# Kernel tuning notes

Measured on AMD Instinct MI355X. Metric: run time of the kernel, lower is better.

Reference implementation:

```python
import jax, jax.numpy as jnp
import numpy as np

M, N, T = 32, 32, 512
H1 = (M + N) * 10 * 8      # 5120
H2 = M * N * 4             # 4096
HID = 1000                 # GRU hidden (hardcoded in module)
EPS = 1e-12


def _l2norm(x):
    # torch.nn.functional.normalize: x / max(||x||_2, eps)
    return x / jnp.maximum(jnp.linalg.norm(x), EPS)


def setup_inputs() -> dict:
    key = jax.random.key(0)
    ks = jax.random.split(key, 16)
    rn = lambda k, shp, s: (jax.random.normal(k, shp, dtype=jnp.float32) * s)
    inp = {
        "y": rn(ks[0], (T, N), 1.0),
        "F": rn(ks[1], (M, M), 0.5 / np.sqrt(M)),   # stable dynamics
        "H": rn(ks[2], (N, M), 1.0 / np.sqrt(M)),
        "m1x0": rn(ks[3], (M,), 1.0),
        "h0": rn(ks[4], (HID,), 1.0),
        "W1": rn(ks[5], (H1, M + N), 1.0 / np.sqrt(M + N)),
        "b1": rn(ks[6], (H1,), 0.01),
        "Wih": rn(ks[7], (3 * HID, H1), 1.0 / np.sqrt(H1)),
        "bih": rn(ks[8], (3 * HID,), 0.01),
        "Whh": rn(ks[9], (3 * HID, HID), 1.0 / np.sqrt(HID)),
        "bhh": rn(ks[10], (3 * HID,), 0.01),
        "W2": rn(ks[11], (H2, HID), 1.0 / np.sqrt(HID)),
        "b2": rn(ks[12], (H2,), 0.01),
        "W3": rn(ks[13], (M * N, H2), 1.0 / np.sqrt(H2)),
        "b3": rn(ks[14], (M * N,), 0.01),
    }
    return inp


def reference(y, F, H, m1x0, h0, W1, b1, Wih, bih, Whh, bhh, W2, b2, W3, b3):
    m, n = F.shape[0], H.shape[0]

    def step(carry, yt):
        m1x_prior, m1x_post, h = carry
        # step_prior
        m1x_prev_prior = m1x_prior
        m1x_prior = F @ m1x_post              # [m]
        m1y = H @ m1x_prior                   # [n]
        # step_KGain_est: features
        dm1x_n = _l2norm(m1x_post - m1x_prev_prior)
        dm1y_n = _l2norm(yt - m1y)
        kin = jnp.concatenate([dm1y_n, dm1x_n])  # [n+m]
        # KGain_step: Linear+ReLU -> single-step GRU -> Linear+ReLU -> Linear
        x = jax.nn.relu(W1 @ kin + b1)        # [H1]
        gi = Wih @ x + bih                    # [3*HID]
        gh = Whh @ h + bhh
        ir, iz, ic = jnp.split(gi, 3)
        hr, hz, hc = jnp.split(gh, 3)
        r = jax.nn.sigmoid(ir + hr)
        z = jax.nn.sigmoid(iz + hz)
        c = jnp.tanh(ic + r * hc)
        h_new = (1.0 - z) * c + z * h         # GRU hidden [HID]
        l2 = jax.nn.relu(W2 @ h_new + b2)     # [H2]
        KG = (W3 @ l2 + b3).reshape(m, n)     # Kalman gain
        # KNet_step: innovation update
        m1x_post_new = m1x_prior + KG @ (yt - m1y)
        return (m1x_prior, m1x_post_new, h_new), m1x_post_new

    init = (m1x0, m1x0, h0)
    _, posts = jax.lax.scan(step, init, y)
    return posts  # [T, m]
```

## Files before the change

### kernel.cpp

```cpp
#include <hip/hip_runtime.h>
#include <cmath>

#define Mdim 32
#define Ndim 32
#define Tsteps 512
#define H1dim 5120
#define H2dim 4096
#define HIDdim 1000
#define NWG 256
#define NTHR 1024
#define POLLER 320

typedef unsigned int u32;
typedef unsigned short u16;
typedef unsigned int u32x4 __attribute__((ext_vector_type(4)));

__device__ u16 g_w2b[H2dim * HIDdim];
__device__ u16 g_w3t[H2dim * Mdim * Ndim];

#define OFF_WIH 0
#define OFF_WHH 122880
#define OFF_UNION 146880
#define OFF_H9 157120
#define OFF_MISC 161640
#define SMEM_BYTES 162560

#define MI_POST 0
#define MI_PRIOR 32
#define MI_INNOV 96
#define MI_KIN 128
#define MI_GI 192
#define MI_GH 204

__device__ __forceinline__ u16 f2bf(float f) {
  u32 u = __float_as_uint(f);
  return (u16)((u + 0x7fffu + ((u >> 16) & 1u)) >> 16);
}
__device__ __forceinline__ float bflo(u32 u) { return __uint_as_float(u << 16); }
__device__ __forceinline__ float bfhi(u32 u) { return __uint_as_float(u & 0xffff0000u); }

__device__ __forceinline__ float dot4(float4 a, float4 b) {
  return a.x * b.x + a.y * b.y + a.z * b.z + a.w * b.w;
}
__device__ __forceinline__ float dot8_bb(uint4 a, uint4 b) {
  float s = 0.f;
  s = fmaf(bflo(a.x), bflo(b.x), s); s = fmaf(bfhi(a.x), bfhi(b.x), s);
  s = fmaf(bflo(a.y), bflo(b.y), s); s = fmaf(bfhi(a.y), bfhi(b.y), s);
  s = fmaf(bflo(a.z), bflo(b.z), s); s = fmaf(bfhi(a.z), bfhi(b.z), s);
  s = fmaf(bflo(a.w), bflo(b.w), s); s = fmaf(bfhi(a.w), bfhi(b.w), s);
  return s;
}
__device__ __forceinline__ float dot8_bf(uint4 a, const float* x8) {
  float s = 0.f;
  s = fmaf(bflo(a.x), x8[0], s); s = fmaf(bfhi(a.x), x8[1], s);
  s = fmaf(bflo(a.y), x8[2], s); s = fmaf(bfhi(a.y), x8[3], s);
  s = fmaf(bflo(a.z), x8[4], s); s = fmaf(bfhi(a.z), x8[5], s);
  s = fmaf(bflo(a.w), x8[6], s); s = fmaf(bfhi(a.w), x8[7], s);
  return s;
}

__device__ __forceinline__ float wave_reduce64(float v) {
#pragma unroll
  for (int off = 32; off >= 1; off >>= 1) v += __shfl_xor(v, off, 64);
  return v;
}

__device__ __forceinline__ uint4 ldg_cg4u(const void* p) {
  uint4 r;
  asm volatile("global_load_dwordx4 %0, %1, off sc0 sc1\n\ts_waitcnt vmcnt(0)"
               : "=v"(r) : "v"(p) : "memory");
  return r;
}
__device__ __forceinline__ void ldg2_cg4(const float* p0, const float* p1,
                                         float4& r0, float4& r1) {
  asm volatile("global_load_dwordx4 %0, %2, off sc0 sc1\n\t"
               "global_load_dwordx4 %1, %3, off sc0 sc1\n\t"
               "s_waitcnt vmcnt(0)"
               : "=&v"(r0), "=&v"(r1) : "v"(p0), "v"(p1) : "memory");
}
__device__ __forceinline__ void stg_cg1(float* p, float v) {
  asm volatile("global_store_dword %0, %1, off sc0 sc1" :: "v"(p), "v"(v) : "memory");
}
__device__ __forceinline__ void stg_cg4u(void* p, u32 a, u32 b, u32 c, u32 d) {
  u32x4 v; v.x = a; v.y = b; v.z = c; v.w = d;
  asm volatile("global_store_dwordx4 %0, %1, off sc0 sc1" :: "v"(p), "v"(v) : "memory");
}

__device__ __forceinline__ void gb_arrive(u32* bar) {
  asm volatile("s_waitcnt vmcnt(0)" ::: "memory");
  __syncthreads();
  if (threadIdx.x == POLLER) {
    u32 g = (u32)blockIdx.x & 15u;
    u32 a = __hip_atomic_fetch_add(bar + g * 16, 1u, __ATOMIC_RELAXED,
                                   __HIP_MEMORY_SCOPE_AGENT);
    if ((a & 15u) == 15u) {
      u32 b = __hip_atomic_fetch_add(bar + 256, 1u, __ATOMIC_RELAXED,
                                     __HIP_MEMORY_SCOPE_AGENT);
      if ((b & 15u) == 15u)
        __hip_atomic_fetch_add(bar + 320, 1u, __ATOMIC_RELAXED,
                               __HIP_MEMORY_SCOPE_AGENT);
    }
  }
}
__device__ __forceinline__ void gb_wait(u32* bar, u32 nb) {
  if (threadIdx.x == POLLER) {
    while (__hip_atomic_load(bar + 320, __ATOMIC_RELAXED,
                             __HIP_MEMORY_SCOPE_AGENT) < nb)
      __builtin_amdgcn_s_sleep(2);
  }
  __syncthreads();
}

__global__ void convert_w2(const float* __restrict__ W2) {
  int i = blockIdx.x * 1024 + threadIdx.x;
  if (i < H2dim * HIDdim) g_w2b[i] = f2bf(W2[i]);
}

__global__ void convert_w3t(const float* __restrict__ W3) {
  __shared__ float tile[32][33];
  int tr = blockIdx.x >> 7;
  int tc = blockIdx.x & 127;
  int r0 = tr * 32, c0 = tc * 32;
  int j = threadIdx.x & 31, i0 = threadIdx.x >> 5;
#pragma unroll
  for (int p = 0; p < 4; ++p) {
    int i = i0 + p * 8;
    tile[i][j] = W3[(size_t)(r0 + i) * H2dim + c0 + j];
  }
  __syncthreads();
#pragma unroll
  for (int p = 0; p < 4; ++p) {
    int i = i0 + p * 8;
    g_w3t[(size_t)(c0 + i) * 1024 + r0 + j] = f2bf(tile[j][i]);
  }
}

__global__ void __launch_bounds__(NTHR)
knet_kernel(const float* __restrict__ y, const float* __restrict__ F,
            const float* __restrict__ Hm, const float* __restrict__ m1x0,
            const float* __restrict__ h0, const float* __restrict__ W1,
            const float* __restrict__ b1, const float* __restrict__ Wih,
            const float* __restrict__ bih, const float* __restrict__ Whh,
            const float* __restrict__ bhh, const float* __restrict__ b2,
            const float* __restrict__ b3, float* __restrict__ out,
            u32* bar, u32* xbt, u32* hbt, float* dpart) {
  extern __shared__ char smem[];
  u16* s_wih = (u16*)(smem + OFF_WIH);
  u16* s_whh = (u16*)(smem + OFF_WHH);
  u16* s_x = (u16*)(smem + OFF_UNION);
  float4* s_red4 = (float4*)(smem + OFF_UNION);
  float* s_redf = (float*)(smem + OFF_UNION);
  float* s_pd = (float*)(smem + OFF_UNION);
  float* s_h9 = (float*)(smem + OFF_H9);
  float* s_m = (float*)(smem + OFF_MISC);
  float* s_post = s_m + MI_POST;
  float* s_prior = s_m + MI_PRIOR;
  float* s_innov = s_m + MI_INNOV;
  float* s_kin = s_m + MI_KIN;
  float* s_gi = s_m + MI_GI;
  float* s_gh = s_m + MI_GH;

  const int tid = threadIdx.x;
  const int w = tid >> 6;
  const int lane = tid & 63;
  const int wg = blockIdx.x;
  const int k0 = wg * 4;
  const bool gru_wg = (wg < 250);
  u32 nb = 0;

  if (gru_wg) {
#pragma unroll 1
    for (int r = 0; r < 12; ++r) {
      const float* src = Wih + (size_t)((r >> 2) * HIDdim + k0 + (r & 3)) * H1dim;
      u16* dst = s_wih + r * H1dim;
      for (int e = tid; e < H1dim; e += NTHR) dst[e] = f2bf(src[e]);
    }
#pragma unroll 1
    for (int r = 0; r < 12; ++r) {
      const float* src = Whh + (size_t)((r >> 2) * HIDdim + k0 + (r & 3)) * HIDdim;
      u16* dst = s_whh + r * HIDdim;
      for (int e = tid; e < HIDdim; e += NTHR) dst[e] = f2bf(src[e]);
    }
  }
  if (tid < 250) {
    float4 hv = ((const float4*)h0)[tid];
    int b0 = tid * 4;
    s_h9[((b0 + 0) >> 3) * 9 + ((b0 + 0) & 7)] = hv.x;
    s_h9[((b0 + 1) >> 3) * 9 + ((b0 + 1) & 7)] = hv.y;
    s_h9[((b0 + 2) >> 3) * 9 + ((b0 + 2) & 7)] = hv.z;
    s_h9[((b0 + 3) >> 3) * 9 + ((b0 + 3) & 7)] = hv.w;
  }
  __syncthreads();

  const int c2 = wg * 16 + w;
  float prior = 0.f, bb = 0.f, yv = 0.f;
  if (w == 0 && lane < 32) {
    prior = m1x0[lane];
    yv = y[lane];
  }

  auto gh_compute = [&]() {
    int base = (w - 12) * 3;
#pragma unroll
    for (int rr = 0; rr < 3; ++rr) {
      int r = base + rr;
      const uint4* wr = (const uint4*)(s_whh + r * HIDdim);
      float acc = dot8_bf(wr[lane], s_h9 + lane * 9);
      if (lane < 61) acc += dot8_bf(wr[lane + 64], s_h9 + (lane + 64) * 9);
      acc = wave_reduce64(acc);
      if (lane == 0) s_gh[r] = acc + bhh[(r >> 2) * HIDdim + k0 + (r & 3)];
    }
  };
  if (gru_wg && w >= 12) gh_compute();

  for (int t = 0; t < Tsteps; ++t) {
    const u32 want = (u32)(t + 1);
    if (t > 0) {
      float4 a0, a1;
      ldg2_cg4(dpart + tid * 4, dpart + (tid + 1024) * 4, a0, a1);
      float4 s;
      s.x = a0.x + a1.x; s.y = a0.y + a1.y; s.z = a0.z + a1.z; s.w = a0.w + a1.w;
#pragma unroll
      for (int off = 8; off <= 32; off <<= 1) {
        s.x += __shfl_xor(s.x, off, 64);
        s.y += __shfl_xor(s.y, off, 64);
        s.z += __shfl_xor(s.z, off, 64);
        s.w += __shfl_xor(s.w, off, 64);
      }
      if (lane < 8) s_red4[w * 8 + lane] = s;
    }
    __syncthreads();
    if (w == 0) {
      float p = 0.f, inn = 0.f;
      float prev = prior;
      if (lane < 32) {
        if (t == 0) {
          p = m1x0[lane];
        } else {
          float dsum = 0.f;
#pragma unroll
          for (int ww = 0; ww < 16; ++ww) dsum += s_redf[ww * 32 + lane];
          p = prior + dsum + bb;
          if (wg == 0) out[(t - 1) * Mdim + lane] = p;
        }
        s_post[lane] = p;
      }
      asm volatile("" ::: "memory");
      if (lane < 32) {
        const float4* Fr = (const float4*)(F + lane * Mdim);
        const float4* pp = (const float4*)s_post;
        float s = 0.f;
#pragma unroll
        for (int j = 0; j < 8; ++j) s += dot4(Fr[j], pp[j]);
        prior = s;
        s_prior[lane] = s;
      }
      asm volatile("" ::: "memory");
      if (lane < 32) {
        const float4* Hr = (const float4*)(Hm + lane * Mdim);
        const float4* pp = (const float4*)s_prior;
        float s = 0.f;
#pragma unroll
        for (int j = 0; j < 8; ++j) s += dot4(Hr[j], pp[j]);
        inn = yv - s;
        s_innov[lane] = inn;
      }
      float vd = __shfl(p, lane & 31, 64) - __shfl(prev, lane & 31, 64);
      float v = (lane < 32) ? inn : vd;
      float sq = v * v;
#pragma unroll
      for (int off = 16; off >= 1; off >>= 1) sq += __shfl_xor(sq, off, 32);
      s_kin[lane] = v / fmaxf(sqrtf(sq), 1e-12f);
    }
    __syncthreads();

    if (w == 0) {
      int r = lane / 3;
      int p = lane - r * 3;
      float acc = 0.f;
      if (r < 20) {
        const float4* Wr = (const float4*)W1 + (size_t)(wg * 20 + r) * 16;
        const float4* kc = (const float4*)s_kin;
#pragma unroll
        for (int c = p; c < 16; c += 3) acc += dot4(Wr[c], kc[c]);
      }
      int rr = (r < 20) ? r : 0;
      float a1v = __shfl(acc, rr * 3 + 1, 64);
      float a2v = __shfl(acc, rr * 3 + 2, 64);
      u32 myval = 0;
      if (r < 20 && p == 0)
        myval = (u32)f2bf(fmaxf(acc + a1v + a2v + b1[wg * 20 + r], 0.f));
      u32 vs[7];
      int q = (lane < 3) ? lane : 0;
#pragma unroll
      for (int s2 = 0; s2 < 7; ++s2) {
        int ridx = q * 7 + s2;
        vs[s2] = __shfl(myval, (ridx < 20 ? ridx : 0) * 3, 64);
      }
      if (lane < 3) {
        stg_cg4u((char*)xbt + (size_t)(wg * 3 + lane) * 16,
                 vs[0] | (vs[1] << 16),
                 vs[2] | (vs[3] << 16),
                 vs[4] | (vs[5] << 16),
                 ((lane == 2) ? 0u : vs[6]) | (want << 16));
      }
    }
    float u;
    uint4 w2a, w2b_;
    {
      const uint4* tr3 = (const uint4*)(g_w3t + (size_t)c2 * 1024);
      uint4 t0 = tr3[2 * lane], t1 = tr3[2 * lane + 1];
      const float* iv = s_innov + 16 * (lane & 1);
      u = dot8_bf(t0, iv) + dot8_bf(t1, iv + 8);
      u += __shfl_xor(u, 1, 64);
      const uint4* w2p = (const uint4*)(g_w2b + (size_t)c2 * HIDdim);
      w2a = w2p[lane];
      w2b_ = (lane < 61) ? w2p[lane + 64] : make_uint4(0u, 0u, 0u, 0u);
    }
    if (gru_wg && tid >= 256) {
      int g = tid - 256;
      int swg = g / 3;
      int q = g - swg * 3;
      const char* gp = (const char*)xbt + (size_t)g * 16;
      uint4 v;
      for (;;) {
        v = ldg_cg4u(gp);
        if ((v.w >> 16) == want) break;
        __builtin_amdgcn_s_sleep(1);
      }
      u16* sx = (u16*)s_x;
      int base = swg * 20 + q * 7;
      sx[base + 0] = (u16)(v.x & 0xffff);
      sx[base + 1] = (u16)(v.x >> 16);
      sx[base + 2] = (u16)(v.y & 0xffff);
      sx[base + 3] = (u16)(v.y >> 16);
      sx[base + 4] = (u16)(v.z & 0xffff);
      sx[base + 5] = (u16)(v.z >> 16);
      if (q != 2) sx[base + 6] = (u16)(v.w & 0xffff);
    }
    __syncthreads();

    if (gru_wg && w < 12) {
      const uint4* wr = (const uint4*)(s_wih + w * H1dim);
      const uint4* xr = (const uint4*)s_x;
      float acc = 0.f;
#pragma unroll
      for (int i = 0; i < 10; ++i) {
        int j = lane + 64 * i;
        acc += dot8_bb(wr[j], xr[j]);
      }
      acc = wave_reduce64(acc);
      if (lane == 0) s_gi[w] = acc + bih[(w >> 2) * HIDdim + k0 + (w & 3)];
    }
    __syncthreads();

    if (gru_wg && w == 0 && lane < 4) {
      int k = k0 + lane;
      float hold = s_h9[(k >> 3) * 9 + (k & 7)];
      float ir = s_gi[lane], iz = s_gi[4 + lane], ic = s_gi[8 + lane];
      float r = 1.f / (1.f + expf(-(ir + s_gh[lane])));
      float z = 1.f / (1.f + expf(-(iz + s_gh[4 + lane])));
      float c_ = tanhf(ic + r * s_gh[8 + lane]);
      float hv = (1.f - z) * c_ + z * hold;
      stg_cg4u((char*)hbt + (size_t)k * 16, __float_as_uint(hv), want, 0u, 0u);
    }
    if (tid < HIDdim) {
      const char* gp = (const char*)hbt + (size_t)tid * 16;
      uint4 v;
      for (;;) {
        v = ldg_cg4u(gp);
        if (v.y == want) break;
        __builtin_amdgcn_s_sleep(1);
      }
      s_h9[(tid >> 3) * 9 + (tid & 7)] = __uint_as_float(v.x);
    }
    __syncthreads();

    {
      float acc = dot8_bf(w2a, s_h9 + lane * 9);
      if (lane < 61) acc += dot8_bf(w2b_, s_h9 + (lane + 64) * 9);
      acc = wave_reduce64(acc);
      float l2c = fmaxf(acc + b2[c2], 0.f);
      if ((lane & 1) == 0) s_pd[w * 32 + (lane >> 1)] = l2c * u;
    }
    __syncthreads();
    if (tid < 32) {
      float pdv = 0.f;
#pragma unroll
      for (int ww = 0; ww < 16; ++ww) pdv += s_pd[ww * 32 + tid];
      stg_cg1(dpart + wg * 32 + tid, pdv);
    }
    ++nb;
    gb_arrive(bar);
    if (gru_wg && w >= 12) gh_compute();
    if (w == 0 && lane < 32) {
      int tn = (t + 1 < Tsteps) ? t + 1 : Tsteps - 1;
      yv = y[tn * Ndim + lane];
      float b = 0.f;
#pragma unroll 8
      for (int j = 0; j < 32; ++j) b = fmaf(b3[lane * 32 + j], s_innov[j], b);
      bb = b;
    }
    gb_wait(bar, nb);
  }

  if (wg == 0) {
    float4 a0, a1;
    ldg2_cg4(dpart + tid * 4, dpart + (tid + 1024) * 4, a0, a1);
    float4 s;
    s.x = a0.x + a1.x; s.y = a0.y + a1.y; s.z = a0.z + a1.z; s.w = a0.w + a1.w;
#pragma unroll
    for (int off = 8; off <= 32; off <<= 1) {
      s.x += __shfl_xor(s.x, off, 64);
      s.y += __shfl_xor(s.y, off, 64);
      s.z += __shfl_xor(s.z, off, 64);
      s.w += __shfl_xor(s.w, off, 64);
    }
    if (lane < 8) s_red4[w * 8 + lane] = s;
    __syncthreads();
    if (w == 0 && lane < 32) {
      float d = 0.f;
#pragma unroll
      for (int ww = 0; ww < 16; ++ww) d += s_redf[ww * 32 + lane];
      out[(Tsteps - 1) * Mdim + lane] = prior + d + bb;
    }
  }
}

extern "C" void kernel_launch(void* const* d_in, const int* in_sizes, int n_in,
                              void* d_out, int out_size, void* d_ws, size_t ws_size,
                              hipStream_t stream) {
  const float* y    = (const float*)d_in[0];
  const float* F    = (const float*)d_in[1];
  const float* Hm   = (const float*)d_in[2];
  const float* m1x0 = (const float*)d_in[3];
  const float* h0   = (const float*)d_in[4];
  const float* W1   = (const float*)d_in[5];
  const float* b1   = (const float*)d_in[6];
  const float* Wih  = (const float*)d_in[7];
  const float* bih  = (const float*)d_in[8];
  const float* Whh  = (const float*)d_in[9];
  const float* bhh  = (const float*)d_in[10];
  const float* W2   = (const float*)d_in[11];
  const float* b2   = (const float*)d_in[12];
  const float* W3   = (const float*)d_in[13];
  const float* b3   = (const float*)d_in[14];
  float* out = (float*)d_out;

  u32* bar   = (u32*)d_ws;
  u32* xbt   = (u32*)((char*)d_ws + 4096);
  u32* hbt   = (u32*)((char*)d_ws + 16384);
  float* dpart = (float*)((char*)d_ws + 32768);

  convert_w2<<<4000, 1024, 0, stream>>>(W2);
  convert_w3t<<<4096, 256, 0, stream>>>(W3);
  hipMemsetAsync(d_ws, 0, 32768, stream);
  hipFuncSetAttribute((const void*)knet_kernel,
                      hipFuncAttributeMaxDynamicSharedMemorySize, SMEM_BYTES);
  void* args[] = {&y, &F, &Hm, &m1x0, &h0, &W1, &b1, &Wih, &bih, &Whh, &bhh,
                  &b2, &b3, &out, &bar, &xbt, &hbt, &dpart};
  hipLaunchCooperativeKernel((const void*)knet_kernel, dim3(NWG), dim3(NTHR),
                             args, SMEM_BYTES, stream);
}
```

Before: 6.385 ms.

## Replace per-workgroup partial buffer with double-buffered global atomic accumulation

Each workgroup now adds its 32 partial KG·innovation sums straight into a small global accumulator using atomics. The accumulator is double-buffered by step parity, and workgroup 0 zeroes the buffer that will be reused. This removes the per-step load of 256×32 partials by every workgroup, along with the shuffle/LDS reduction and one barrier. It adds 8192 atomics per step contending on 32 addresses and relies on ordering between the zeroing stores and the global barrier. The barrier poll sleep is also shortened.

```diff
diff --git a/kernel.cpp b/kernel.cpp
--- a/kernel.cpp
+++ b/kernel.cpp
@@ -71,15 +71,11 @@
                : "=v"(r) : "v"(p) : "memory");
   return r;
 }
-__device__ __forceinline__ void ldg2_cg4(const float* p0, const float* p1,
-                                         float4& r0, float4& r1) {
-  asm volatile("global_load_dwordx4 %0, %2, off sc0 sc1\n\t"
-               "global_load_dwordx4 %1, %3, off sc0 sc1\n\t"
-               "s_waitcnt vmcnt(0)"
-               : "=&v"(r0), "=&v"(r1) : "v"(p0), "v"(p1) : "memory");
-}
-__device__ __forceinline__ void stg_cg1(float* p, float v) {
-  asm volatile("global_store_dword %0, %1, off sc0 sc1" :: "v"(p), "v"(v) : "memory");
+__device__ __forceinline__ float ldg_cg1f(const float* p) {
+  float r;
+  asm volatile("global_load_dword %0, %1, off sc0 sc1\n\ts_waitcnt vmcnt(0)"
+               : "=v"(r) : "v"(p) : "memory");
+  return r;
 }
 __device__ __forceinline__ void stg_cg4u(void* p, u32 a, u32 b, u32 c, u32 d) {
   u32x4 v; v.x = a; v.y = b; v.z = c; v.w = d;
@@ -106,7 +102,7 @@
   if (threadIdx.x == POLLER) {
     while (__hip_atomic_load(bar + 320, __ATOMIC_RELAXED,
                              __HIP_MEMORY_SCOPE_AGENT) < nb)
-      __builtin_amdgcn_s_sleep(2);
+      __builtin_amdgcn_s_sleep(1);
   }
   __syncthreads();
 }
@@ -143,13 +139,11 @@
             const float* __restrict__ bih, const float* __restrict__ Whh,
             const float* __restrict__ bhh, const float* __restrict__ b2,
             const float* __restrict__ b3, float* __restrict__ out,
-            u32* bar, u32* xbt, u32* hbt, float* dpart) {
+            u32* bar, u32* xbt, u32* hbt, float* acc) {
   extern __shared__ char smem[];
   u16* s_wih = (u16*)(smem + OFF_WIH);
   u16* s_whh = (u16*)(smem + OFF_WHH);
   u16* s_x = (u16*)(smem + OFF_UNION);
-  float4* s_red4 = (float4*)(smem + OFF_UNION);
-  float* s_redf = (float*)(smem + OFF_UNION);
   float* s_pd = (float*)(smem + OFF_UNION);
   float* s_h9 = (float*)(smem + OFF_H9);
   float* s_m = (float*)(smem + OFF_MISC);
@@ -205,31 +199,18 @@
     for (int rr = 0; rr < 3; ++rr) {
       int r = base + rr;
       const uint4* wr = (const uint4*)(s_whh + r * HIDdim);
-      float acc = dot8_bf(wr[lane], s_h9 + lane * 9);
-      if (lane < 61) acc += dot8_bf(wr[lane + 64], s_h9 + (lane + 64) * 9);
-      acc = wave_reduce64(acc);
-      if (lane == 0) s_gh[r] = acc + bhh[(r >> 2) * HIDdim + k0 + (r & 3)];
+      float acc_ = dot8_bf(wr[lane], s_h9 + lane * 9);
+      if (lane < 61) acc_ += dot8_bf(wr[lane + 64], s_h9 + (lane + 64) * 9);
+      acc_ = wave_reduce64(acc_);
+      if (lane == 0) s_gh[r] = acc_ + bhh[(r >> 2) * HIDdim + k0 + (r & 3)];
     }
   };
   if (gru_wg && w >= 12) gh_compute();
 
   for (int t = 0; t < Tsteps; ++t) {
     const u32 want = (u32)(t + 1);
-    if (t > 0) {
-      float4 a0, a1;
-      ldg2_cg4(dpart + tid * 4, dpart + (tid + 1024) * 4, a0, a1);
-      float4 s;
-      s.x = a0.x + a1.x; s.y = a0.y + a1.y; s.z = a0.z + a1.z; s.w = a0.w + a1.w;
-#pragma unroll
-      for (int off = 8; off <= 32; off <<= 1) {
-        s.x += __shfl_xor(s.x, off, 64);
-        s.y += __shfl_xor(s.y, off, 64);
-        s.z += __shfl_xor(s.z, off, 64);
-        s.w += __shfl_xor(s.w, off, 64);
-      }
-      if (lane < 8) s_red4[w * 8 + lane] = s;
-    }
-    __syncthreads();
+    const int parR = (t + 1) & 1;
+    const int parW = t & 1;
     if (w == 0) {
       float p = 0.f, inn = 0.f;
       float prev = prior;
@@ -237,10 +218,8 @@
         if (t == 0) {
           p = m1x0[lane];
         } else {
-          float dsum = 0.f;
-#pragma unroll
-          for (int ww = 0; ww < 16; ++ww) dsum += s_redf[ww * 32 + lane];
-          p = prior + dsum + bb;
+          float d = ldg_cg1f(acc + parR * 32 + lane);
+          p = prior + d + bb;
           if (wg == 0) out[(t - 1) * Mdim + lane] = p;
         }
         s_post[lane] = p;
@@ -277,19 +256,19 @@
     if (w == 0) {
       int r = lane / 3;
       int p = lane - r * 3;
-      float acc = 0.f;
+      float acc_ = 0.f;
       if (r < 20) {
         const float4* Wr = (const float4*)W1 + (size_t)(wg * 20 + r) * 16;
         const float4* kc = (const float4*)s_kin;
 #pragma unroll
-        for (int c = p; c < 16; c += 3) acc += dot4(Wr[c], kc[c]);
+        for (int c = p; c < 16; c += 3) acc_ += dot4(Wr[c], kc[c]);
       }
       int rr = (r < 20) ? r : 0;
-      float a1v = __shfl(acc, rr * 3 + 1, 64);
-      float a2v = __shfl(acc, rr * 3 + 2, 64);
+      float a1v = __shfl(acc_, rr * 3 + 1, 64);
+      float a2v = __shfl(acc_, rr * 3 + 2, 64);
       u32 myval = 0;
       if (r < 20 && p == 0)
-        myval = (u32)f2bf(fmaxf(acc + a1v + a2v + b1[wg * 20 + r], 0.f));
+        myval = (u32)f2bf(fmaxf(acc_ + a1v + a2v + b1[wg * 20 + r], 0.f));
       u32 vs[7];
       int q = (lane < 3) ? lane : 0;
 #pragma unroll
@@ -340,17 +319,29 @@
     }
     __syncthreads();
 
+    if (wg == 0 && tid == 1016) {
+      float* z = acc + parR * 32;
+      stg_cg4u(z, 0u, 0u, 0u, 0u);
+      stg_cg4u(z + 4, 0u, 0u, 0u, 0u);
+      stg_cg4u(z + 8, 0u, 0u, 0u, 0u);
+      stg_cg4u(z + 12, 0u, 0u, 0u, 0u);
+      stg_cg4u(z + 16, 0u, 0u, 0u, 0u);
+      stg_cg4u(z + 20, 0u, 0u, 0u, 0u);
+      stg_cg4u(z + 24, 0u, 0u, 0u, 0u);
+      stg_cg4u(z + 28, 0u, 0u, 0u, 0u);
+    }
+
     if (gru_wg && w < 12) {
       const uint4* wr = (const uint4*)(s_wih + w * H1dim);
       const uint4* xr = (const uint4*)s_x;
-      float acc = 0.f;
+      float acc_ = 0.f;
 #pragma unroll
       for (int i = 0; i < 10; ++i) {
         int j = lane + 64 * i;
-        acc += dot8_bb(wr[j], xr[j]);
-      }
-      acc = wave_reduce64(acc);
-      if (lane == 0) s_gi[w] = acc + bih[(w >> 2) * HIDdim + k0 + (w & 3)];
+        acc_ += dot8_bb(wr[j], xr[j]);
+      }
+      acc_ = wave_reduce64(acc_);
+      if (lane == 0) s_gi[w] = acc_ + bih[(w >> 2) * HIDdim + k0 + (w & 3)];
     }
     __syncthreads();
 
@@ -377,10 +368,10 @@
     __syncthreads();
 
     {
-      float acc = dot8_bf(w2a, s_h9 + lane * 9);
-      if (lane < 61) acc += dot8_bf(w2b_, s_h9 + (lane + 64) * 9);
-      acc = wave_reduce64(acc);
-      float l2c = fmaxf(acc + b2[c2], 0.f);
+      float acc_ = dot8_bf(w2a, s_h9 + lane * 9);
+      if (lane < 61) acc_ += dot8_bf(w2b_, s_h9 + (lane + 64) * 9);
+      acc_ = wave_reduce64(acc_);
+      float l2c = fmaxf(acc_ + b2[c2], 0.f);
       if ((lane & 1) == 0) s_pd[w * 32 + (lane >> 1)] = l2c * u;
     }
     __syncthreads();
@@ -388,7 +379,8 @@
       float pdv = 0.f;
 #pragma unroll
       for (int ww = 0; ww < 16; ++ww) pdv += s_pd[ww * 32 + tid];
-      stg_cg1(dpart + wg * 32 + tid, pdv);
+      __hip_atomic_fetch_add(acc + parW * 32 + tid, pdv, __ATOMIC_RELAXED,
+                             __HIP_MEMORY_SCOPE_AGENT);
     }
     ++nb;
     gb_arrive(bar);
@@ -404,26 +396,9 @@
     gb_wait(bar, nb);
   }
 
-  if (wg == 0) {
-    float4 a0, a1;
-    ldg2_cg4(dpart + tid * 4, dpart + (tid + 1024) * 4, a0, a1);
-    float4 s;
-    s.x = a0.x + a1.x; s.y = a0.y + a1.y; s.z = a0.z + a1.z; s.w = a0.w + a1.w;
-#pragma unroll
-    for (int off = 8; off <= 32; off <<= 1) {
-      s.x += __shfl_xor(s.x, off, 64);
-      s.y += __shfl_xor(s.y, off, 64);
-      s.z += __shfl_xor(s.z, off, 64);
-      s.w += __shfl_xor(s.w, off, 64);
-    }
-    if (lane < 8) s_red4[w * 8 + lane] = s;
-    __syncthreads();
-    if (w == 0 && lane < 32) {
-      float d = 0.f;
-#pragma unroll
-      for (int ww = 0; ww < 16; ++ww) d += s_redf[ww * 32 + lane];
-      out[(Tsteps - 1) * Mdim + lane] = prior + d + bb;
-    }
+  if (wg == 0 && w == 0 && lane < 32) {
+    float d = ldg_cg1f(acc + ((Tsteps - 1) & 1) * 32 + lane);
+    out[(Tsteps - 1) * Mdim + lane] = prior + d + bb;
   }
 }
 
@@ -448,17 +423,17 @@
   float* out = (float*)d_out;
 
   u32* bar   = (u32*)d_ws;
-  u32* xbt   = (u32*)((char*)d_ws + 4096);
-  u32* hbt   = (u32*)((char*)d_ws + 16384);
-  float* dpart = (float*)((char*)d_ws + 32768);
+  float* acc = (float*)((char*)d_ws + 4096);
+  u32* xbt   = (u32*)((char*)d_ws + 8192);
+  u32* hbt   = (u32*)((char*)d_ws + 20480);
 
   convert_w2<<<4000, 1024, 0, stream>>>(W2);
   convert_w3t<<<4096, 256, 0, stream>>>(W3);
-  hipMemsetAsync(d_ws, 0, 32768, stream);
+  hipMemsetAsync(d_ws, 0, 36864, stream);
   hipFuncSetAttribute((const void*)knet_kernel,
                       hipFuncAttributeMaxDynamicSharedMemorySize, SMEM_BYTES);
   void* args[] = {&y, &F, &Hm, &m1x0, &h0, &W1, &b1, &Wih, &bih, &Whh, &bhh,
-                  &b2, &b3, &out, &bar, &xbt, &hbt, &dpart};
+                  &b2, &b3, &out, &bar, &xbt, &hbt, &acc};
   hipLaunchCooperativeKernel((const void*)knet_kernel, dim3(NWG), dim3(NTHR),
                              args, SMEM_BYTES, stream);
 }
```

Measured after the change: 7.370 ms. 1.15x slower.
